# Performance work log

Measured on AMD Instinct MI355X. Metric: run time of the kernel, lower is better.

The kernel has to match this reference:

```python
import jax, jax.numpy as jnp
import numpy as np
import math

B, S, D, H, R = 4, 4096, 1024, 16, 256
DK = D // H

def setup_inputs() -> dict:
    key = jax.random.key(0)
    ks = jax.random.split(key, 16)
    def lin(k, fan_in, fan_out):
        # torch Linear default init: U(-1/sqrt(fan_in), 1/sqrt(fan_in))
        bound = 1.0 / math.sqrt(fan_in)
        kw, kb = jax.random.split(k)
        W = jax.random.uniform(kw, (fan_out, fan_in), jnp.float32, -bound, bound)
        b = jax.random.uniform(kb, (fan_out,), jnp.float32, -bound, bound)
        return W, b
    Wq, bq = lin(ks[0], D, D)
    Wk, bk = lin(ks[1], D, D)
    Wv, bv = lin(ks[2], D, D)
    Wo, bo = lin(ks[3], D, D)
    # xavier_uniform over last two dims (S, R)
    xav = math.sqrt(6.0 / (S + R))
    E = jax.random.uniform(ks[4], (H, S, R), jnp.float32, -xav, xav)
    F = jax.random.uniform(ks[5], (H, S, R), jnp.float32, -xav, xav)
    query = jax.random.normal(ks[6], (B, S, D), jnp.float32)
    key_ = jax.random.normal(ks[7], (B, S, D), jnp.float32)
    value = jax.random.normal(ks[8], (B, S, D), jnp.float32)
    return {"query": query, "key": key_, "value": value,
            "Wq": Wq, "bq": bq, "Wk": Wk, "bk": bk, "Wv": Wv, "bv": bv,
            "Wo": Wo, "bo": bo, "E": E, "F": F}

def _split_heads(x):
    # [B, S, D] -> [B, H, S, DK]
    b, s, _ = x.shape
    return x.reshape(b, s, H, DK).transpose(0, 2, 1, 3)

def reference(query, key, value, Wq, bq, Wk, bk, Wv, bv, Wo, bo, E, F):
    q = _split_heads(query @ Wq.T + bq)   # [B,H,S,DK]
    k = _split_heads(key @ Wk.T + bk)
    v = _split_heads(value @ Wv.T + bv)
    # key^T @ E : [B,H,DK,S] @ [H,S,R] -> [B,H,DK,R]
    kp = jnp.einsum('bhsd,hsr->bhdr', k, E)
    vp = jnp.einsum('bhsd,hsr->bhdr', v, F)
    attn = jnp.einsum('bhsd,bhdr->bhsr', q, kp) / math.sqrt(DK)
    attn = jax.nn.softmax(attn, axis=-1)  # [B,H,S,R]
    out = jnp.einsum('bhsr,bhdr->bhsd', attn, vp)  # [B,H,S,DK]
    out = out.transpose(0, 2, 1, 3).reshape(query.shape[0], -1, D)
    return out @ Wo.T + bo
```

## Files before the change

### kernel.cpp

```cpp
#include <hip/hip_runtime.h>


typedef __bf16 bf16;
typedef bf16 bf16x8 __attribute__((ext_vector_type(8)));
typedef bf16 bf16x4 __attribute__((ext_vector_type(4)));
typedef float f32x4 __attribute__((ext_vector_type(4)));

constexpr int BB = 4, SS = 4096, DD = 1024, HH = 16, RR = 256, DK = 64;

#define QSCALE 0.1803368801111204f

__device__ __forceinline__ void gl2lds16(const void* g, void* l, int lane)
{
#if __has_builtin(__builtin_amdgcn_global_load_lds)
    auto gp = reinterpret_cast<const __attribute__((address_space(1))) void*>(
        reinterpret_cast<uintptr_t>(g));
    auto lp = reinterpret_cast<__attribute__((address_space(3))) void*>(
        reinterpret_cast<uintptr_t>(l));
    __builtin_amdgcn_global_load_lds(gp, lp, 16, 0, 0);
    (void)lane;
#else
    *(bf16x8*)((char*)l + lane * 16) = *(const bf16x8*)g;
#endif
}

#define VMW3  asm volatile("s_waitcnt vmcnt(3)" ::: "memory")
#define VMW0  asm volatile("s_waitcnt vmcnt(0)" ::: "memory")
#define LGKM0 asm volatile("s_waitcnt lgkmcnt(0)" ::: "memory")

__global__ void cvt_f32_bf16(const float* __restrict__ in, bf16* __restrict__ out, int n)
{
    int i = (blockIdx.x * 256 + threadIdx.x) * 8;
    if (i < n) {
        float4 v0 = *(const float4*)(in + i);
        float4 v1 = *(const float4*)(in + i + 4);
        bf16x8 h;
        h[0] = (bf16)v0.x; h[1] = (bf16)v0.y; h[2] = (bf16)v0.z; h[3] = (bf16)v0.w;
        h[4] = (bf16)v1.x; h[5] = (bf16)v1.y; h[6] = (bf16)v1.z; h[7] = (bf16)v1.w;
        *(bf16x8*)(out + i) = h;
    }
}

__global__ void transpose_cvt(const float* __restrict__ in, bf16* __restrict__ out,
                              int rows, int cols)
{
    __shared__ float t[64][65];
    const float* I = in + (size_t)blockIdx.z * rows * cols;
    bf16* O = out + (size_t)blockIdx.z * rows * cols;
    int c0 = blockIdx.x * 64, r0 = blockIdx.y * 64;
    int tx = threadIdx.x, ty = threadIdx.y;
#pragma unroll
    for (int i = ty; i < 64; i += 4)
        t[i][tx] = I[(size_t)(r0 + i) * cols + c0 + tx];
    __syncthreads();
#pragma unroll
    for (int i = ty; i < 64; i += 4)
        O[(size_t)(c0 + i) * rows + r0 + tx] = (bf16)t[tx][i];
}

template <bool OUT_F32>
__global__ __launch_bounds__(512, 4) void gemm_bt(const bf16* __restrict__ A,
                                                  const bf16* __restrict__ W,
                                                  const float* __restrict__ bias,
                                                  void* __restrict__ Cp,
                                                  int M, int N, int K, float oscale)
{
    __shared__ bf16 As[2][256][32];
    __shared__ bf16 Bs[2][128][32];
    const int tid = threadIdx.x, wv = tid >> 6, lane = tid & 63;
    const int g = lane >> 4, lr = lane & 15;

    const int nwg = gridDim.x;
    const int cpx = nwg >> 3;
    const int bid = blockIdx.x;
    const int swz = (bid & 7) * cpx + (bid >> 3);
    const int gx = N >> 7;
    const int mt = swz / gx, nt = swz % gx;
    const int m0 = mt * 256, n0 = nt * 128;
    const int wm = (wv >> 1) * 64, wn = (wv & 1) * 64;

    const int srow = lane >> 2;
    const int scol = ((lane & 3) ^ ((lane >> 4) & 3)) * 8;

    f32x4 acc[4][4] = {};

    auto stageA = [&](int buf, int tk) {
#pragma unroll
        for (int s2 = 0; s2 < 2; ++s2) {
            int c = wv * 2 + s2;
            gl2lds16(A + (size_t)(m0 + c * 16 + srow) * 1024 + tk * 32 + scol,
                     &As[buf][c * 16][0], lane);
        }
    };
    auto stageB = [&](int buf, int tk) {
        gl2lds16(W + (size_t)(n0 + wv * 16 + srow) * 1024 + tk * 32 + scol,
                 &Bs[buf][wv * 16][0], lane);
    };

#define PHK(PB, STAGE_STMT, VM_STMT)                                             \
    {                                                                            \
        const int so = (g ^ (lr >> 2)) << 4;                                     \
        bf16x8 aF[4], bF[4];                                                     \
        _Pragma("unroll") for (int mm = 0; mm < 4; ++mm)                         \
            aF[mm] = *(const bf16x8*)((const char*)&As[PB][wm + mm * 16 + lr][0] + so); \
        _Pragma("unroll") for (int nn = 0; nn < 4; ++nn)                         \
            bF[nn] = *(const bf16x8*)((const char*)&Bs[PB][wn + nn * 16 + lr][0] + so); \
        LGKM0;                                                                   \
        __builtin_amdgcn_s_barrier();                 \
        STAGE_STMT;                                     \
        VM_STMT;                                             \
        __builtin_amdgcn_s_barrier();                   \
        __builtin_amdgcn_sched_barrier(0);                                       \
        __builtin_amdgcn_s_setprio(1);                                           \
        _Pragma("unroll") for (int mm = 0; mm < 4; ++mm) {                       \
            _Pragma("unroll") for (int nn = 0; nn < 4; ++nn) {                   \
                acc[mm][nn] = __builtin_amdgcn_mfma_f32_16x16x32_bf16(           \
                    aF[mm], bF[nn], acc[mm][nn], 0, 0, 0); } }                   \
        __builtin_amdgcn_s_setprio(0);                                           \
    }

    stageA(0, 0); stageB(0, 0);
    stageA(1, 1); stageB(1, 1);
    VMW3;
    __builtin_amdgcn_s_barrier();

#pragma unroll 1
    for (int t = 0; t < 30; ++t) {
        const int pb = t & 1;
        PHK(pb, { stageA(pb, t + 2); stageB(pb, t + 2); }, VMW3);
    }
    PHK(0, (void)0, VMW0);
    PHK(1, (void)0, (void)0);
#undef PHK

    float bv[4];
#pragma unroll
    for (int n = 0; n < 4; ++n) bv[n] = bias[n0 + wn + n * 16 + lr];

    if constexpr (OUT_F32) {
#pragma unroll
        for (int n = 0; n < 4; ++n) {
            int col = n0 + wn + n * 16 + lr;
#pragma unroll
            for (int m = 0; m < 4; ++m) {
                int row = m0 + wm + m * 16 + 4 * g;
#pragma unroll
                for (int i = 0; i < 4; ++i)
                    ((float*)Cp)[(size_t)(row + i) * N + col] = (acc[m][n][i] + bv[n]) * oscale;
            }
        }
    } else {
        char* myb = (char*)&As[0][0][0] + wv * 4096;
#pragma unroll
        for (int mh = 0; mh < 2; ++mh) {
#pragma unroll
            for (int mm = 0; mm < 2; ++mm)
#pragma unroll
                for (int n = 0; n < 4; ++n) {
                    int colb = (n * 16 + lr) * 2;
#pragma unroll
                    for (int i = 0; i < 4; ++i) {
                        int row = mm * 16 + 4 * g + i;
                        *(bf16*)(myb + row * 128 + (colb ^ ((row & 7) << 4))) =
                            (bf16)((acc[mh * 2 + mm][n][i] + bv[n]) * oscale);
                    }
                }
            __builtin_amdgcn_wave_barrier();
            bf16* Cb = (bf16*)Cp + (size_t)(m0 + wm + mh * 32) * N + n0 + wn;
#pragma unroll
            for (int it = 0; it < 4; ++it) {
                int r = it * 8 + (lane >> 3);
                int sl = lane & 7;
                bf16x8 vv = *(const bf16x8*)(myb + r * 128 + ((sl ^ (r & 7)) << 4));
                *(bf16x8*)(Cb + (size_t)r * N + sl * 8) = vv;
            }
            __builtin_amdgcn_wave_barrier();
        }
    }
}

__global__ __launch_bounds__(256) void kpvp_gemm(const bf16* __restrict__ X,
                                                 const bf16* __restrict__ P,
                                                 float* __restrict__ out)
{
    __shared__ bf16 Ak[64][40];
    __shared__ bf16 Bs[256][32];
    const int b = blockIdx.z, h = blockIdx.y;
    const int s0 = blockIdx.x * 512;
    const int tid = threadIdx.x, wv = tid >> 6, lane = tid & 63;
    const int g = lane >> 4, lr = lane & 15;
    const int lrow = lane >> 2, lcol = (lane & 3) * 8;
    const bf16* Pg = P + ((size_t)h * RR + wv * 64 + lrow) * SS + lcol;
    f32x4 acc[4][4] = {};

    for (int kt = 0; kt < 512; kt += 32) {
        const int sb = s0 + kt;
        __syncthreads();
#pragma unroll
        for (int j = 0; j < 4; ++j)
            gl2lds16(Pg + (size_t)(j * 16) * SS + sb, &Bs[wv * 64 + j * 16][0], lane);
        {
            int sl = tid >> 3, dblk = (tid & 7) * 8;
            bf16x8 v = *(const bf16x8*)(X + ((size_t)b * SS + sb + sl) * DD + h * DK + dblk);
#pragma unroll
            for (int j = 0; j < 8; ++j) Ak[dblk + j][sl] = v[j];
        }
        __syncthreads();

        bf16x8 a[4], bb[4];
#pragma unroll
        for (int m = 0; m < 4; ++m) a[m] = *(const bf16x8*)&Ak[m * 16 + lr][g * 8];
#pragma unroll
        for (int n = 0; n < 4; ++n) bb[n] = *(const bf16x8*)&Bs[wv * 64 + n * 16 + lr][g * 8];
#pragma unroll
        for (int m = 0; m < 4; ++m)
#pragma unroll
            for (int n = 0; n < 4; ++n)
                acc[m][n] = __builtin_amdgcn_mfma_f32_16x16x32_bf16(a[m], bb[n], acc[m][n], 0, 0, 0);
    }

    float* o = out + ((size_t)(b * HH + h)) * DK * RR;
#pragma unroll
    for (int m = 0; m < 4; ++m)
#pragma unroll
        for (int n = 0; n < 4; ++n) {
            int r = wv * 64 + n * 16 + lr;
#pragma unroll
            for (int i = 0; i < 4; ++i)
                atomicAdd(o + (size_t)(m * 16 + 4 * g + i) * RR + r, acc[m][n][i]);
        }
}

__global__ __launch_bounds__(512) void attn_fused(const bf16* __restrict__ qb,
                                                  const bf16* __restrict__ kpt,
                                                  const bf16* __restrict__ vpb,
                                                  bf16* __restrict__ ctx)
{
    __shared__ bf16 KPs[256][72];
    __shared__ bf16 VPs[64][264];
    __shared__ bf16 Ps[8][16][264];
    const int b = blockIdx.z, h = blockIdx.y, qt = blockIdx.x;
    const int tid = threadIdx.x, wv = tid >> 6, lane = tid & 63;
    const int g = lane >> 4, lr = lane & 15;
    const bf16* kph = kpt + ((size_t)(b * HH + h)) * RR * DK;
    const bf16* vph = vpb + ((size_t)(b * HH + h)) * DK * RR;

#pragma unroll
    for (int p = 0; p < 4; ++p) {
        int f = p * 512 + tid;
        *(bf16x8*)&KPs[f >> 3][(f & 7) * 8] = *(const bf16x8*)(kph + (size_t)f * 8);
        *(bf16x8*)&VPs[f >> 5][(f & 31) * 8] = *(const bf16x8*)(vph + (size_t)f * 8);
    }

    const bf16* qbase = qb + (size_t)b * SS * DD + h * DK;
    int row0 = qt * 1024 + wv * 16;
    bf16x8 aq0 = *(const bf16x8*)(qbase + (size_t)(row0 + lr) * DD + g * 8);
    bf16x8 aq1 = *(const bf16x8*)(qbase + (size_t)(row0 + lr) * DD + 32 + g * 8);
    __syncthreads();

    for (int it = 0; it < 8; ++it) {
        f32x4 acc[16] = {};
        __builtin_amdgcn_s_setprio(1);
#pragma unroll
        for (int nf = 0; nf < 16; ++nf) {
            bf16x8 b0 = *(const bf16x8*)&KPs[nf * 16 + lr][g * 8];
            bf16x8 b1 = *(const bf16x8*)&KPs[nf * 16 + lr][32 + g * 8];
            acc[nf] = __builtin_amdgcn_mfma_f32_16x16x32_bf16(aq0, b0, acc[nf], 0, 0, 0);
            acc[nf] = __builtin_amdgcn_mfma_f32_16x16x32_bf16(aq1, b1, acc[nf], 0, 0, 0);
        }
        __builtin_amdgcn_s_setprio(0);

        bf16x8 aqn0 = aq0, aqn1 = aq1;
        if (it < 7) {
            const bf16* qr = qbase + (size_t)(row0 + 128 + lr) * DD;
            aqn0 = *(const bf16x8*)(qr + g * 8);
            aqn1 = *(const bf16x8*)(qr + 32 + g * 8);
        }

        float rs[4];
#pragma unroll
        for (int i = 0; i < 4; ++i) {
            float s = 0.f;
#pragma unroll
            for (int nf = 0; nf < 16; ++nf) {
                float pv = exp2f(acc[nf][i]);
                acc[nf][i] = pv;
                s += pv;
            }
#pragma unroll
            for (int msk = 1; msk < 16; msk <<= 1) s += __shfl_xor(s, msk, 64);
            rs[i] = 1.f / s;
        }

#pragma unroll
        for (int nf = 0; nf < 16; ++nf)
#pragma unroll
            for (int i = 0; i < 4; ++i)
                Ps[wv][4 * g + i][nf * 16 + lr] = (bf16)acc[nf][i];
        __builtin_amdgcn_wave_barrier();

        f32x4 o[4] = {};
        __builtin_amdgcn_s_setprio(1);
#pragma unroll
        for (int ks = 0; ks < 8; ++ks) {
            bf16x8 pa = *(const bf16x8*)&Ps[wv][lr][ks * 32 + g * 8];
#pragma unroll
            for (int n = 0; n < 4; ++n) {
                bf16x8 vb = *(const bf16x8*)&VPs[n * 16 + lr][ks * 32 + g * 8];
                o[n] = __builtin_amdgcn_mfma_f32_16x16x32_bf16(pa, vb, o[n], 0, 0, 0);
            }
        }
        __builtin_amdgcn_s_setprio(0);
        __builtin_amdgcn_wave_barrier();

#pragma unroll
        for (int n = 0; n < 4; ++n)
#pragma unroll
            for (int i = 0; i < 4; ++i)
                Ps[wv][4 * g + i][n * 16 + lr] = (bf16)(o[n][i] * rs[i]);
        __builtin_amdgcn_wave_barrier();
        bf16* crow = ctx + (size_t)(b * SS + row0) * DD + h * DK;
#pragma unroll
        for (int p = 0; p < 2; ++p) {
            int r = p * 8 + (lane >> 3), c = (lane & 7) * 8;
            bf16x8 ov = *(const bf16x8*)&Ps[wv][r][c];
            *(bf16x8*)(crow + (size_t)r * DD + c) = ov;
        }
        __builtin_amdgcn_wave_barrier();

        aq0 = aqn0; aq1 = aqn1;
        row0 += 128;
    }
}

extern "C" void kernel_launch(void* const* d_in, const int* in_sizes, int n_in,
                              void* d_out, int out_size, void* d_ws, size_t ws_size,
                              hipStream_t stream)
{
    const float* query = (const float*)d_in[0];
    const float* key   = (const float*)d_in[1];
    const float* value = (const float*)d_in[2];
    const float* Wq = (const float*)d_in[3];  const float* bq = (const float*)d_in[4];
    const float* Wk = (const float*)d_in[5];  const float* bk = (const float*)d_in[6];
    const float* Wv = (const float*)d_in[7];  const float* bv = (const float*)d_in[8];
    const float* Wo = (const float*)d_in[9];  const float* bo = (const float*)d_in[10];
    const float* E  = (const float*)d_in[11];
    const float* F  = (const float*)d_in[12];

    char* w = (char*)d_ws;
    size_t off = 0;
    auto alloc = [&](size_t bytes) -> char* {
        char* p = w + off;
        off += (bytes + 255) & ~(size_t)255;
        return p;
    };

    const size_t DW   = (size_t)DD * DD;
    const size_t BSD  = (size_t)BB * SS * DD;
    const size_t HRS  = (size_t)HH * RR * SS;
    const size_t BHDR = (size_t)BB * HH * DK * RR;

    bf16* wqb = (bf16*)alloc(DW * 2);
    bf16* wkb = (bf16*)alloc(DW * 2);
    bf16* wvb = (bf16*)alloc(DW * 2);
    bf16* wob = (bf16*)alloc(DW * 2);
    bf16* ebt = (bf16*)alloc(HRS * 2);
    bf16* fbt = (bf16*)alloc(HRS * 2);
    bf16* qin = (bf16*)alloc(BSD * 2);
    bf16* kin = (bf16*)alloc(BSD * 2);
    bf16* vin = (bf16*)alloc(BSD * 2);
    bf16* qbuf = (bf16*)alloc(BSD * 2);
    bf16* kbuf = (bf16*)alloc(BSD * 2);
    bf16* vbuf = (bf16*)alloc(BSD * 2);
    if (off > ws_size) return;

    float* kpf  = (float*)qin;
    float* vpf  = kpf + BHDR;
    bf16*  kpt  = (bf16*)kin;
    bf16*  vpbb = kpt + BHDR;
    bf16*  ctx  = (bf16*)vin;

    cvt_f32_bf16<<<(int)(DW / 2048), 256, 0, stream>>>(Wq, wqb, (int)DW);
    cvt_f32_bf16<<<(int)(DW / 2048), 256, 0, stream>>>(Wk, wkb, (int)DW);
    cvt_f32_bf16<<<(int)(DW / 2048), 256, 0, stream>>>(Wv, wvb, (int)DW);
    cvt_f32_bf16<<<(int)(DW / 2048), 256, 0, stream>>>(Wo, wob, (int)DW);
    cvt_f32_bf16<<<(int)(BSD / 2048), 256, 0, stream>>>(query, qin, (int)BSD);
    cvt_f32_bf16<<<(int)(BSD / 2048), 256, 0, stream>>>(key,   kin, (int)BSD);
    cvt_f32_bf16<<<(int)(BSD / 2048), 256, 0, stream>>>(value, vin, (int)BSD);

    dim3 tb(64, 4);
    transpose_cvt<<<dim3(RR / 64, SS / 64, HH), tb, 0, stream>>>(E, ebt, SS, RR);
    transpose_cvt<<<dim3(RR / 64, SS / 64, HH), tb, 0, stream>>>(F, fbt, SS, RR);

    const int nwg = ((BB * SS) / 256) * (DD / 128);
    gemm_bt<false><<<nwg, 512, 0, stream>>>(qin, wqb, bq, qbuf, BB * SS, DD, DD, QSCALE);
    gemm_bt<false><<<nwg, 512, 0, stream>>>(kin, wkb, bk, kbuf, BB * SS, DD, DD, 1.0f);
    gemm_bt<false><<<nwg, 512, 0, stream>>>(vin, wvb, bv, vbuf, BB * SS, DD, DD, 1.0f);

    hipMemsetAsync(kpf, 0, BHDR * 4 * 2, stream);
    kpvp_gemm<<<dim3(SS / 512, HH, BB), 256, 0, stream>>>(kbuf, ebt, kpf);
    kpvp_gemm<<<dim3(SS / 512, HH, BB), 256, 0, stream>>>(vbuf, fbt, vpf);

    transpose_cvt<<<dim3(RR / 64, DK / 64, BB * HH), tb, 0, stream>>>(kpf, kpt, DK, RR);
    cvt_f32_bf16<<<(int)(BHDR / 2048), 256, 0, stream>>>(vpf, vpbb, (int)BHDR);

    attn_fused<<<dim3(SS / 1024, HH, BB), 512, 0, stream>>>(qbuf, kpt, vpbb, ctx);

    gemm_bt<true><<<nwg, 512, 0, stream>>>(ctx, wob, bo, d_out, BB * SS, DD, DD, 1.0f);
}
```

Measured before the change: 445.6 us.

## Read fp32 E/F directly in kpvp GEMM and software-pipeline attention QK

```diff
diff --git a/kernel.cpp b/kernel.cpp
--- a/kernel.cpp
+++ b/kernel.cpp
@@ -180,38 +180,45 @@
 }
 
 __global__ __launch_bounds__(256) void kpvp_gemm(const bf16* __restrict__ X,
-                                                 const bf16* __restrict__ P,
+                                                 const float* __restrict__ E,
                                                  float* __restrict__ out)
 {
     __shared__ bf16 Ak[64][40];
-    __shared__ bf16 Bs[256][32];
     const int b = blockIdx.z, h = blockIdx.y;
     const int s0 = blockIdx.x * 512;
     const int tid = threadIdx.x, wv = tid >> 6, lane = tid & 63;
     const int g = lane >> 4, lr = lane & 15;
-    const int lrow = lane >> 2, lcol = (lane & 3) * 8;
-    const bf16* Pg = P + ((size_t)h * RR + wv * 64 + lrow) * SS + lcol;
+    const float* Eh = E + (size_t)h * SS * RR;
+    const int rbase = wv * 64 + lr;
     f32x4 acc[4][4] = {};
 
     for (int kt = 0; kt < 512; kt += 32) {
         const int sb = s0 + kt;
         __syncthreads();
-#pragma unroll
-        for (int j = 0; j < 4; ++j)
-            gl2lds16(Pg + (size_t)(j * 16) * SS + sb, &Bs[wv * 64 + j * 16][0], lane);
+        float ef[4][8];
+        const float* Eb = Eh + (size_t)(sb + g * 8) * RR + rbase;
+#pragma unroll
+        for (int n = 0; n < 4; ++n)
+#pragma unroll
+            for (int j = 0; j < 8; ++j)
+                ef[n][j] = Eb[(size_t)j * RR + n * 16];
         {
             int sl = tid >> 3, dblk = (tid & 7) * 8;
             bf16x8 v = *(const bf16x8*)(X + ((size_t)b * SS + sb + sl) * DD + h * DK + dblk);
 #pragma unroll
             for (int j = 0; j < 8; ++j) Ak[dblk + j][sl] = v[j];
         }
+        bf16x8 bb[4];
+#pragma unroll
+        for (int n = 0; n < 4; ++n)
+#pragma unroll
+            for (int j = 0; j < 8; ++j)
+                bb[n][j] = (bf16)ef[n][j];
         __syncthreads();
 
-        bf16x8 a[4], bb[4];
+        bf16x8 a[4];
 #pragma unroll
         for (int m = 0; m < 4; ++m) a[m] = *(const bf16x8*)&Ak[m * 16 + lr][g * 8];
-#pragma unroll
-        for (int n = 0; n < 4; ++n) bb[n] = *(const bf16x8*)&Bs[wv * 64 + n * 16 + lr][g * 8];
 #pragma unroll
         for (int m = 0; m < 4; ++m)
 #pragma unroll
@@ -253,84 +260,98 @@
     }
 
     const bf16* qbase = qb + (size_t)b * SS * DD + h * DK;
-    int row0 = qt * 1024 + wv * 16;
-    bf16x8 aq0 = *(const bf16x8*)(qbase + (size_t)(row0 + lr) * DD + g * 8);
-    bf16x8 aq1 = *(const bf16x8*)(qbase + (size_t)(row0 + lr) * DD + 32 + g * 8);
+    const int row0 = qt * 1024 + wv * 16;
+
+    bf16x8 qa0 = *(const bf16x8*)(qbase + (size_t)(row0 + lr) * DD + g * 8);
+    bf16x8 qa1 = *(const bf16x8*)(qbase + (size_t)(row0 + lr) * DD + 32 + g * 8);
     __syncthreads();
 
-    for (int it = 0; it < 8; ++it) {
-        f32x4 acc[16] = {};
-        __builtin_amdgcn_s_setprio(1);
-#pragma unroll
-        for (int nf = 0; nf < 16; ++nf) {
-            bf16x8 b0 = *(const bf16x8*)&KPs[nf * 16 + lr][g * 8];
-            bf16x8 b1 = *(const bf16x8*)&KPs[nf * 16 + lr][32 + g * 8];
-            acc[nf] = __builtin_amdgcn_mfma_f32_16x16x32_bf16(aq0, b0, acc[nf], 0, 0, 0);
-            acc[nf] = __builtin_amdgcn_mfma_f32_16x16x32_bf16(aq1, b1, acc[nf], 0, 0, 0);
-        }
-        __builtin_amdgcn_s_setprio(0);
-
-        bf16x8 aqn0 = aq0, aqn1 = aq1;
-        if (it < 7) {
-            const bf16* qr = qbase + (size_t)(row0 + 128 + lr) * DD;
-            aqn0 = *(const bf16x8*)(qr + g * 8);
-            aqn1 = *(const bf16x8*)(qr + 32 + g * 8);
-        }
-
-        float rs[4];
-#pragma unroll
-        for (int i = 0; i < 4; ++i) {
-            float s = 0.f;
-#pragma unroll
-            for (int nf = 0; nf < 16; ++nf) {
-                float pv = exp2f(acc[nf][i]);
-                acc[nf][i] = pv;
-                s += pv;
-            }
-#pragma unroll
-            for (int msk = 1; msk < 16; msk <<= 1) s += __shfl_xor(s, msk, 64);
-            rs[i] = 1.f / s;
-        }
-
-#pragma unroll
-        for (int nf = 0; nf < 16; ++nf)
-#pragma unroll
-            for (int i = 0; i < 4; ++i)
-                Ps[wv][4 * g + i][nf * 16 + lr] = (bf16)acc[nf][i];
-        __builtin_amdgcn_wave_barrier();
-
-        f32x4 o[4] = {};
-        __builtin_amdgcn_s_setprio(1);
-#pragma unroll
-        for (int ks = 0; ks < 8; ++ks) {
-            bf16x8 pa = *(const bf16x8*)&Ps[wv][lr][ks * 32 + g * 8];
-#pragma unroll
-            for (int n = 0; n < 4; ++n) {
-                bf16x8 vb = *(const bf16x8*)&VPs[n * 16 + lr][ks * 32 + g * 8];
-                o[n] = __builtin_amdgcn_mfma_f32_16x16x32_bf16(pa, vb, o[n], 0, 0, 0);
-            }
-        }
-        __builtin_amdgcn_s_setprio(0);
-        __builtin_amdgcn_wave_barrier();
-
-#pragma unroll
-        for (int n = 0; n < 4; ++n)
-#pragma unroll
-            for (int i = 0; i < 4; ++i)
-                Ps[wv][4 * g + i][n * 16 + lr] = (bf16)(o[n][i] * rs[i]);
-        __builtin_amdgcn_wave_barrier();
-        bf16* crow = ctx + (size_t)(b * SS + row0) * DD + h * DK;
-#pragma unroll
-        for (int p = 0; p < 2; ++p) {
-            int r = p * 8 + (lane >> 3), c = (lane & 7) * 8;
-            bf16x8 ov = *(const bf16x8*)&Ps[wv][r][c];
-            *(bf16x8*)(crow + (size_t)r * DD + c) = ov;
-        }
-        __builtin_amdgcn_wave_barrier();
-
-        aq0 = aqn0; aq1 = aqn1;
-        row0 += 128;
-    }
+    f32x4 pA[16] = {}, pB[16] = {};
+#pragma unroll
+    for (int nf = 0; nf < 16; ++nf) {
+        bf16x8 b0 = *(const bf16x8*)&KPs[nf * 16 + lr][g * 8];
+        bf16x8 b1 = *(const bf16x8*)&KPs[nf * 16 + lr][32 + g * 8];
+        pA[nf] = __builtin_amdgcn_mfma_f32_16x16x32_bf16(qa0, b0, pA[nf], 0, 0, 0);
+        pA[nf] = __builtin_amdgcn_mfma_f32_16x16x32_bf16(qa1, b1, pA[nf], 0, 0, 0);
+    }
+    {
+        const bf16* qr = qbase + (size_t)(row0 + 128 + lr) * DD;
+        qa0 = *(const bf16x8*)(qr + g * 8);
+        qa1 = *(const bf16x8*)(qr + 32 + g * 8);
+    }
+
+#define AITER(PC, PN, IT)                                                        \
+    {                                                                            \
+                                                        \
+        bf16x8 qn0 = qa0, qn1 = qa1;                                             \
+        if ((IT) < 6) {                                                          \
+            const bf16* qr = qbase + (size_t)(row0 + ((IT) + 2) * 128 + lr) * DD;\
+            qn0 = *(const bf16x8*)(qr + g * 8);                                  \
+            qn1 = *(const bf16x8*)(qr + 32 + g * 8);                             \
+        }                                                                        \
+             \
+        if ((IT) < 7) {                                                          \
+            _Pragma("unroll") for (int nf = 0; nf < 16; ++nf) {                  \
+                bf16x8 b0 = *(const bf16x8*)&KPs[nf * 16 + lr][g * 8];           \
+                bf16x8 b1 = *(const bf16x8*)&KPs[nf * 16 + lr][32 + g * 8];      \
+                PN[nf] = __builtin_amdgcn_mfma_f32_16x16x32_bf16(qa0, b0, PN[nf], 0, 0, 0); \
+                PN[nf] = __builtin_amdgcn_mfma_f32_16x16x32_bf16(qa1, b1, PN[nf], 0, 0, 0); \
+            }                                                                    \
+        }                                                                        \
+                                                              \
+        float rs[4];                                                             \
+        _Pragma("unroll") for (int i = 0; i < 4; ++i) {                          \
+            float s = 0.f;                                                       \
+            _Pragma("unroll") for (int nf = 0; nf < 16; ++nf) {                  \
+                float pv = exp2f(PC[nf][i]);                                     \
+                PC[nf][i] = pv;                                                  \
+                s += pv;                                                         \
+            }                                                                    \
+            _Pragma("unroll") for (int msk = 1; msk < 16; msk <<= 1)             \
+                s += __shfl_xor(s, msk, 64);                                     \
+            rs[i] = 1.f / s;                                                     \
+        }                                                                        \
+        _Pragma("unroll") for (int nf = 0; nf < 16; ++nf)                        \
+            _Pragma("unroll") for (int i = 0; i < 4; ++i)                        \
+                Ps[wv][4 * g + i][nf * 16 + lr] = (bf16)PC[nf][i];               \
+        __builtin_amdgcn_wave_barrier();                                         \
+        f32x4 o[4] = {};                                                         \
+        __builtin_amdgcn_s_setprio(1);                                           \
+        _Pragma("unroll") for (int ks = 0; ks < 8; ++ks) {                       \
+            bf16x8 pa = *(const bf16x8*)&Ps[wv][lr][ks * 32 + g * 8];            \
+            _Pragma("unroll") for (int n = 0; n < 4; ++n) {                      \
+                bf16x8 vb = *(const bf16x8*)&VPs[n * 16 + lr][ks * 32 + g * 8];  \
+                o[n] = __builtin_amdgcn_mfma_f32_16x16x32_bf16(pa, vb, o[n], 0, 0, 0); \
+            }                                                                    \
+        }                                                                        \
+        __builtin_amdgcn_s_setprio(0);                                           \
+        __builtin_amdgcn_wave_barrier();                                         \
+        _Pragma("unroll") for (int n = 0; n < 4; ++n)                            \
+            _Pragma("unroll") for (int i = 0; i < 4; ++i)                        \
+                Ps[wv][4 * g + i][n * 16 + lr] = (bf16)(o[n][i] * rs[i]);        \
+        __builtin_amdgcn_wave_barrier();                                         \
+        bf16* crow = ctx + (size_t)(b * SS + row0 + (IT) * 128) * DD + h * DK;   \
+        _Pragma("unroll") for (int p = 0; p < 2; ++p) {                          \
+            int r = p * 8 + (lane >> 3), c = (lane & 7) * 8;                     \
+            bf16x8 ov = *(const bf16x8*)&Ps[wv][r][c];                           \
+            *(bf16x8*)(crow + (size_t)r * DD + c) = ov;                          \
+        }                                                                        \
+        __builtin_amdgcn_wave_barrier();                                         \
+                     \
+        _Pragma("unroll") for (int nf = 0; nf < 16; ++nf)                        \
+            PC[nf] = (f32x4){0.f, 0.f, 0.f, 0.f};                                \
+        qa0 = qn0; qa1 = qn1;                                                    \
+    }
+
+    AITER(pA, pB, 0);
+    AITER(pB, pA, 1);
+    AITER(pA, pB, 2);
+    AITER(pB, pA, 3);
+    AITER(pA, pB, 4);
+    AITER(pB, pA, 5);
+    AITER(pA, pB, 6);
+    AITER(pB, pA, 7);
+#undef AITER
 }
 
 extern "C" void kernel_launch(void* const* d_in, const int* in_sizes, int n_in,
@@ -357,15 +378,12 @@
 
     const size_t DW   = (size_t)DD * DD;
     const size_t BSD  = (size_t)BB * SS * DD;
-    const size_t HRS  = (size_t)HH * RR * SS;
     const size_t BHDR = (size_t)BB * HH * DK * RR;
 
     bf16* wqb = (bf16*)alloc(DW * 2);
     bf16* wkb = (bf16*)alloc(DW * 2);
     bf16* wvb = (bf16*)alloc(DW * 2);
     bf16* wob = (bf16*)alloc(DW * 2);
-    bf16* ebt = (bf16*)alloc(HRS * 2);
-    bf16* fbt = (bf16*)alloc(HRS * 2);
     bf16* qin = (bf16*)alloc(BSD * 2);
     bf16* kin = (bf16*)alloc(BSD * 2);
     bf16* vin = (bf16*)alloc(BSD * 2);
@@ -388,19 +406,16 @@
     cvt_f32_bf16<<<(int)(BSD / 2048), 256, 0, stream>>>(key,   kin, (int)BSD);
     cvt_f32_bf16<<<(int)(BSD / 2048), 256, 0, stream>>>(value, vin, (int)BSD);
 
-    dim3 tb(64, 4);
-    transpose_cvt<<<dim3(RR / 64, SS / 64, HH), tb, 0, stream>>>(E, ebt, SS, RR);
-    transpose_cvt<<<dim3(RR / 64, SS / 64, HH), tb, 0, stream>>>(F, fbt, SS, RR);
-
     const int nwg = ((BB * SS) / 256) * (DD / 128);
     gemm_bt<false><<<nwg, 512, 0, stream>>>(qin, wqb, bq, qbuf, BB * SS, DD, DD, QSCALE);
     gemm_bt<false><<<nwg, 512, 0, stream>>>(kin, wkb, bk, kbuf, BB * SS, DD, DD, 1.0f);
     gemm_bt<false><<<nwg, 512, 0, stream>>>(vin, wvb, bv, vbuf, BB * SS, DD, DD, 1.0f);
 
     hipMemsetAsync(kpf, 0, BHDR * 4 * 2, stream);
-    kpvp_gemm<<<dim3(SS / 512, HH, BB), 256, 0, stream>>>(kbuf, ebt, kpf);
-    kpvp_gemm<<<dim3(SS / 512, HH, BB), 256, 0, stream>>>(vbuf, fbt, vpf);
-
+    kpvp_gemm<<<dim3(SS / 512, HH, BB), 256, 0, stream>>>(kbuf, E, kpf);
+    kpvp_gemm<<<dim3(SS / 512, HH, BB), 256, 0, stream>>>(vbuf, F, vpf);
+
+    dim3 tb(64, 4);
     transpose_cvt<<<dim3(RR / 64, DK / 64, BB * HH), tb, 0, stream>>>(kpf, kpt, DK, RR);
     cvt_f32_bf16<<<(int)(BHDR / 2048), 256, 0, stream>>>(vpf, vpbb, (int)BHDR);
 
```

Result: faster. 387.7 us (-13.0%).
